# Kernel tuning notes

Hardware: AMD Instinct MI355X
Metric: run time of the kernel (lower is better)

Reference implementation:

```python
import jax, jax.numpy as jnp
import numpy as np

N_NODES = 100000
N_EDGES = 1600000
FEAT = 128
HID = 128
CLASSES = 10
GRAPHS = 64


def gcn_conv(x, W, b, src, dst, n):
    # PyG GCNConv: h = x @ W; add self-loops; symmetric deg^{-1/2} norm; scatter-add; + bias
    h = x @ W
    src_f = jnp.concatenate([src, jnp.arange(n, dtype=src.dtype)])
    dst_f = jnp.concatenate([dst, jnp.arange(n, dtype=dst.dtype)])
    deg = jax.ops.segment_sum(jnp.ones_like(dst_f, dtype=h.dtype), dst_f, num_segments=n)
    dinv = jax.lax.rsqrt(jnp.where(deg > 0, deg, 1.0))
    norm = dinv[src_f] * dinv[dst_f]              # [E+N]
    msg = h[src_f] * norm[:, None]                # gather + scale
    out = jax.ops.segment_sum(msg, dst_f, num_segments=n)  # scatter-add
    return out + b


def global_mean_pool(x, batch, num_graphs):
    s = jax.ops.segment_sum(x, batch, num_segments=num_graphs)
    cnt = jax.ops.segment_sum(jnp.ones_like(batch, dtype=x.dtype), batch, num_segments=num_graphs)
    return s / jnp.maximum(cnt, 1.0)[:, None]


def setup_inputs() -> dict:
    key = jax.random.key(0)
    ks = jax.random.split(key, 10)
    x = jax.random.normal(ks[0], (N_NODES, FEAT), dtype=jnp.float32)
    edge_index = jax.random.randint(ks[1], (2, N_EDGES), 0, N_NODES, dtype=jnp.int64)
    batch = jnp.sort(jax.random.randint(ks[2], (N_NODES,), 0, GRAPHS, dtype=jnp.int64))
    def glorot(k, fi, fo):
        s = float(np.sqrt(6.0 / (fi + fo)))
        return jax.random.uniform(k, (fi, fo), jnp.float32, -s, s)
    return {
        "x": x, "edge_index": edge_index, "batch": batch,
        "W1": glorot(ks[3], FEAT, HID), "b1": jnp.zeros((HID,), jnp.float32),
        "W2": glorot(ks[4], HID, HID), "b2": jnp.zeros((HID,), jnp.float32),
        "W3": glorot(ks[5], HID, HID), "b3": jnp.zeros((HID,), jnp.float32),
        "Wlin": glorot(ks[6], HID, CLASSES), "blin": jnp.zeros((CLASSES,), jnp.float32),
    }


def reference(x, edge_index, batch, W1, b1, W2, b2, W3, b3, Wlin, blin):
    src, dst = edge_index[0], edge_index[1]
    n = x.shape[0]
    h = jax.nn.relu(gcn_conv(x, W1, b1, src, dst, n))
    h = jax.nn.relu(gcn_conv(h, W2, b2, src, dst, n))
    h = gcn_conv(h, W3, b3, src, dst, n)
    emb = global_mean_pool(h, batch, GRAPHS)      # [GRAPHS, HID]
    # dropout(p=0.5) is identity in eval mode
    logits = emb @ Wlin + blin                    # [GRAPHS, CLASSES]
    return logits, jnp.squeeze(emb)
```

## Files before the change

### kernel.cpp

```cpp
#include <hip/hip_runtime.h>
#include <hip/hip_bf16.h>
#include <stdint.h>

typedef unsigned int uint32;
typedef __attribute__((ext_vector_type(8))) short short8;
typedef __attribute__((ext_vector_type(4))) float float4v;

#define FEAT 128
#define NGRAPH 64
#define SBLK 256
#define STHR 256
#define SSEG 2
#define GB   256
#define NBK  512

__device__ __forceinline__ float bf2f_lo(uint32 v) {
    union { uint32 i; float f; } u; u.i = v << 16; return u.f;
}
__device__ __forceinline__ float bf2f_hi(uint32 v) {
    union { uint32 i; float f; } u; u.i = v & 0xffff0000u; return u.f;
}
__device__ __forceinline__ unsigned short f2bf(float f) {
    uint32 u = __builtin_bit_cast(uint32, f);
    uint32 r = (u + 0x7fffu + ((u >> 16) & 1u)) >> 16;
    return (unsigned short)r;
}
__device__ __forceinline__ uint32 f2bf2(float lo, float hi) {
    return (uint32)f2bf(lo) | ((uint32)f2bf(hi) << 16);
}


__global__ void k_bhist(const int* __restrict__ dst, int* __restrict__ bhist, int E) {
    __shared__ int h[NBK];
    int t = threadIdx.x, blk = blockIdx.x;
    for (int b = t; b < NBK; b += 256) h[b] = 0;
    __syncthreads();
    int chunk = (E + GB - 1) / GB;
    int lo = blk * chunk, hi = min(lo + chunk, E);
    for (int e = lo + t; e < hi; e += 256)
        atomicAdd(&h[dst[e] >> 8], 1);
    __syncthreads();
    for (int b = t; b < NBK; b += 256) bhist[blk * NBK + b] = h[b];
}

__global__ void k_boffs(int* __restrict__ bhist, int* __restrict__ bbase) {
    __shared__ int sc[NBK];
    int t = threadIdx.x;
    int tot = 0;
    for (int blk = 0; blk < GB; blk++) {
        int v = bhist[blk * NBK + t];
        bhist[blk * NBK + t] = tot;
        tot += v;
    }
    sc[t] = tot;
    __syncthreads();
    for (int off = 1; off < NBK; off <<= 1) {
        int v = (t >= off) ? sc[t - off] : 0;
        __syncthreads();
        sc[t] += v;
        __syncthreads();
    }
    bbase[t] = sc[t] - tot;
    if (t == NBK - 1) bbase[NBK] = sc[t];
}

__global__ void k_bscat(const int* __restrict__ src, const int* __restrict__ dst,
                        const int* __restrict__ bhist, const int* __restrict__ bbase,
                        uint32* __restrict__ ebuf, int E) {
    __shared__ int cur[NBK];
    int t = threadIdx.x, blk = blockIdx.x;
    for (int b = t; b < NBK; b += 256) cur[b] = bbase[b] + bhist[blk * NBK + b];
    __syncthreads();
    int chunk = (E + GB - 1) / GB;
    int lo = blk * chunk, hi = min(lo + chunk, E);
    for (int e = lo + t; e < hi; e += 256) {
        int d = dst[e], s = src[e];
        int b = d >> 8;
        int p = atomicAdd(&cur[b], 1);
        ebuf[p] = ((uint32)s << 8) | (uint32)(d & 255);
    }
}

__global__ void k_count2(const uint32* __restrict__ ebuf, const int* __restrict__ bbase,
                         int* __restrict__ counts, int N) {
    __shared__ int h[256];
    int t = threadIdx.x, b = blockIdx.x;
    h[t] = 0;
    __syncthreads();
    int e0 = bbase[b], e1 = bbase[b + 1];
    for (int e = e0 + t; e < e1; e += 256)
        atomicAdd(&h[ebuf[e] & 255u], 1);
    __syncthreads();
    int node = b * 256 + t;
    if (node < N) counts[node] = h[t];
}

__global__ void k_fill2(const uint32* __restrict__ ebuf, const int* __restrict__ bbase,
                        const int* __restrict__ rowp, int* __restrict__ csrc, int N) {
    __shared__ int cur[256];
    int t = threadIdx.x, b = blockIdx.x;
    int node = b * 256 + t;
    cur[t] = (node < N) ? rowp[node] : 0;
    __syncthreads();
    int e0 = bbase[b], e1 = bbase[b + 1];
    for (int e = e0 + t; e < e1; e += 256) {
        uint32 v = ebuf[e];
        int p = atomicAdd(&cur[v & 255u], 1);
        csrc[p] = (int)(v >> 8);
    }
}

__global__ void k_dinv(const int* __restrict__ counts, float* __restrict__ dinv, int N) {
    int i = blockIdx.x * blockDim.x + threadIdx.x;
    if (i < N) dinv[i] = rsqrtf((float)counts[i] + 1.0f);
}

__global__ void k_scan_a(const int* __restrict__ counts, int* __restrict__ tbase,
                         int* __restrict__ bsum, int N) {
    __shared__ int sc[STHR];
    int t = threadIdx.x, b = blockIdx.x;
    int g = b * STHR + t;
    int lo = g * SSEG;
    int s = 0;
#pragma unroll
    for (int j = 0; j < SSEG; j++) {
        int i = lo + j;
        if (i < N) s += counts[i];
    }
    sc[t] = s;
    __syncthreads();
    for (int off = 1; off < STHR; off <<= 1) {
        int v = (t >= off) ? sc[t - off] : 0;
        __syncthreads();
        sc[t] += v;
        __syncthreads();
    }
    tbase[g] = sc[t] - s;
    if (t == STHR - 1) bsum[b] = sc[t];
}

__global__ void k_scan_b(const int* __restrict__ bsum, int* __restrict__ bbase2,
                         int* __restrict__ rowp, int N) {
    __shared__ int sc[SBLK];
    int t = threadIdx.x;
    int s = bsum[t];
    sc[t] = s;
    __syncthreads();
    for (int off = 1; off < SBLK; off <<= 1) {
        int v = (t >= off) ? sc[t - off] : 0;
        __syncthreads();
        sc[t] += v;
        __syncthreads();
    }
    bbase2[t] = sc[t] - s;
    if (t == SBLK - 1) rowp[N] = sc[t];
}

__global__ void k_scan_c(const int* __restrict__ counts, const int* __restrict__ tbase,
                         const int* __restrict__ bbase2, int* __restrict__ rowp, int N) {
    int t = threadIdx.x, b = blockIdx.x;
    int g = b * STHR + t;
    int base = bbase2[b] + tbase[g];
    int lo = g * SSEG;
#pragma unroll
    for (int j = 0; j < SSEG; j++) {
        int i = lo + j;
        if (i < N) { rowp[i] = base; base += counts[i]; }
    }
}

__global__ void k_cast(const float* __restrict__ X, uint32* __restrict__ Xb, long n2) {
    long i = (long)blockIdx.x * blockDim.x + threadIdx.x;
    long stride = (long)gridDim.x * blockDim.x;
    for (; i < n2; i += stride) {
        float2 v = *(const float2*)(X + 2 * i);
        Xb[i] = f2bf2(v.x, v.y);
    }
}

__global__ void k_wswz(const float* __restrict__ W, unsigned short* __restrict__ out) {
    int e = blockIdx.x * blockDim.x + threadIdx.x;
    if (e >= 2048) return;
    int kt = e >> 9, ct = (e >> 6) & 7, lane = e & 63;
    int krow = kt * 32 + (lane >> 4) * 8;
    int col = ct * 16 + (lane & 15);
#pragma unroll
    for (int j = 0; j < 8; j++)
        out[e * 8 + j] = f2bf(W[(krow + j) * FEAT + col]);
}

__global__ void k_gemm(const uint32* __restrict__ Xb,
                       const unsigned short* __restrict__ Wswz,
                       const float* __restrict__ dinv,
                       unsigned short* __restrict__ Hb, int N) {
    __shared__ unsigned short Wl[FEAT * FEAT];
    {
        const uint4* Wg = (const uint4*)Wswz;
        uint4* Ws = (uint4*)Wl;
        for (int i = threadIdx.x; i < 2048; i += 256) Ws[i] = Wg[i];
    }
    __syncthreads();

    int wave = threadIdx.x >> 6, lane = threadIdx.x & 63;
    int r0 = (blockIdx.x * 4 + wave) * 16;
    if (r0 >= N) return;
    int m = lane & 15, q = lane >> 4;

    int arow = r0 + m; if (arow >= N) arow = N - 1;
    const short8* Arow = (const short8*)((const unsigned short*)Xb + (long)arow * FEAT);
    short8 a0 = Arow[q + 0];
    short8 a1 = Arow[4 + q];
    short8 a2 = Arow[8 + q];
    short8 a3 = Arow[12 + q];

    const short8* Bl = (const short8*)Wl;
    float4v acc[8];
#pragma unroll
    for (int ct = 0; ct < 8; ct++) acc[ct] = (float4v){0.f, 0.f, 0.f, 0.f};

#pragma unroll
    for (int ct = 0; ct < 8; ct++) {
        acc[ct] = __builtin_amdgcn_mfma_f32_16x16x32_bf16(a0, Bl[(0 * 8 + ct) * 64 + lane], acc[ct], 0, 0, 0);
        acc[ct] = __builtin_amdgcn_mfma_f32_16x16x32_bf16(a1, Bl[(1 * 8 + ct) * 64 + lane], acc[ct], 0, 0, 0);
        acc[ct] = __builtin_amdgcn_mfma_f32_16x16x32_bf16(a2, Bl[(2 * 8 + ct) * 64 + lane], acc[ct], 0, 0, 0);
        acc[ct] = __builtin_amdgcn_mfma_f32_16x16x32_bf16(a3, Bl[(3 * 8 + ct) * 64 + lane], acc[ct], 0, 0, 0);
    }

    float ds[4];
#pragma unroll
    for (int reg = 0; reg < 4; reg++) {
        int row = r0 + q * 4 + reg;
        ds[reg] = (row < N) ? dinv[row] : 0.f;
    }
#pragma unroll
    for (int ct = 0; ct < 8; ct++) {
#pragma unroll
        for (int reg = 0; reg < 4; reg++) {
            int row = r0 + q * 4 + reg;
            if (row < N) Hb[(long)row * FEAT + ct * 16 + m] = f2bf(acc[ct][reg] * ds[reg]);
        }
    }
}

__global__ void k_agg(const uint32* __restrict__ Hb,
                      const int* __restrict__ rowp, const int* __restrict__ csrc,
                      const float* __restrict__ dinv, const float* __restrict__ bias,
                      uint32* __restrict__ OUTb, int N, int relu) {
    int wave = threadIdx.x >> 6, lane = threadIdx.x & 63;
    int i = blockIdx.x * 4 + wave;
    if (i >= N) return;
    float di = dinv[i];
    uint32 hv = Hb[(long)i * 64 + lane];
    float ax = bf2f_lo(hv), ay = bf2f_hi(hv);
    int e0 = rowp[i], e1 = rowp[i + 1];
    int e = e0;
    for (; e + 8 <= e1; e += 8) {
        int   s[8];
        uint32 h[8];
#pragma unroll
        for (int j = 0; j < 8; j++) s[j] = csrc[e + j];
#pragma unroll
        for (int j = 0; j < 8; j++) h[j] = Hb[(long)s[j] * 64 + lane];
#pragma unroll
        for (int j = 0; j < 8; j++) {
            ax += bf2f_lo(h[j]);
            ay += bf2f_hi(h[j]);
        }
    }
    {
        int   s[8];
        uint32 h[8];
        int r = e1 - e;
#pragma unroll
        for (int j = 0; j < 8; j++)
            if (j < r) s[j] = csrc[e + j];
#pragma unroll
        for (int j = 0; j < 8; j++)
            if (j < r) h[j] = Hb[(long)s[j] * 64 + lane];
#pragma unroll
        for (int j = 0; j < 8; j++)
            if (j < r) { ax += bf2f_lo(h[j]); ay += bf2f_hi(h[j]); }
    }
    ax = ax * di + bias[2 * lane];
    ay = ay * di + bias[2 * lane + 1];
    if (relu) { ax = fmaxf(ax, 0.f); ay = fmaxf(ay, 0.f); }
    OUTb[(long)i * 64 + lane] = f2bf2(ax, ay);
}

__global__ void k_pool(const uint32* __restrict__ Gb, const int* __restrict__ batch,
                       float* __restrict__ pool, int* __restrict__ cntg, int N) {
    int t = threadIdx.x;
    int nb = gridDim.x;
    int chunk = (N + nb - 1) / nb;
    int lo = blockIdx.x * chunk, hi = min(lo + chunk, N);
    if (lo >= hi) return;
    float ax = 0.f, ay = 0.f;
    int cnt = 0;
    int cg = batch[lo];
    for (int i = lo; i < hi; i++) {
        int g = batch[i];
        if (g != cg) {
            atomicAdd(&pool[cg * FEAT + 2 * t], ax);
            atomicAdd(&pool[cg * FEAT + 2 * t + 1], ay);
            if (t == 0) atomicAdd(&cntg[cg], cnt);
            ax = ay = 0.f; cnt = 0; cg = g;
        }
        uint32 v = Gb[(long)i * 64 + t];
        ax += bf2f_lo(v); ay += bf2f_hi(v);
        cnt++;
    }
    atomicAdd(&pool[cg * FEAT + 2 * t], ax);
    atomicAdd(&pool[cg * FEAT + 2 * t + 1], ay);
    if (t == 0) atomicAdd(&cntg[cg], cnt);
}

__global__ void k_final(const float* __restrict__ pool, const int* __restrict__ cntg,
                        const float* __restrict__ Wlin, const float* __restrict__ blin,
                        float* __restrict__ out) {
    __shared__ float es[FEAT];
    int g = blockIdx.x, t = threadIdx.x;
    float c = (float)max(cntg[g], 1);
    float e = pool[g * FEAT + t] / c;
    es[t] = e;
    out[NGRAPH * 10 + g * FEAT + t] = e;
    __syncthreads();
    if (t < 10) {
        float a = blin[t];
        for (int k = 0; k < FEAT; k++)
            a += es[k] * Wlin[k * 10 + t];
        out[g * 10 + t] = a;
    }
}

extern "C" void kernel_launch(void* const* d_in, const int* in_sizes, int n_in,
                              void* d_out, int out_size, void* d_ws, size_t ws_size,
                              hipStream_t stream) {
    const float* x    = (const float*)d_in[0];
    const int*   ei   = (const int*)d_in[1];
    const int*   batch= (const int*)d_in[2];
    const float* W1   = (const float*)d_in[3];
    const float* b1   = (const float*)d_in[4];
    const float* W2   = (const float*)d_in[5];
    const float* b2   = (const float*)d_in[6];
    const float* W3   = (const float*)d_in[7];
    const float* b3   = (const float*)d_in[8];
    const float* Wlin = (const float*)d_in[9];
    const float* blin = (const float*)d_in[10];

    const int N = in_sizes[2];
    const int E = in_sizes[1] / 2;
    const int* src = ei;
    const int* dst = ei + E;
    const int NB = (N + 255) >> 8;

    char* w = (char*)d_ws;
    auto take = [&](size_t bytes) {
        char* p = w;
        w += (bytes + 255) & ~(size_t)255;
        return p;
    };
    int*    counts = (int*)   take((size_t)N * 4);
    float*  dinv   = (float*) take((size_t)N * 4);
    int*    rowp   = (int*)   take((size_t)(N + 1) * 4);
    int*    csrc   = (int*)   take((size_t)E * 4);
    uint32* ebuf   = (uint32*)take((size_t)E * 4);
    int*    bhist  = (int*)   take((size_t)GB * NBK * 4);
    int*    bbase  = (int*)   take((size_t)(NBK + 1) * 4);
    uint32* xb     = (uint32*)take((size_t)N * FEAT * 2);
    uint32* hbuf   = (uint32*)take((size_t)N * FEAT * 2);
    uint32* gbuf   = (uint32*)take((size_t)N * FEAT * 2);
    unsigned short* w1s = (unsigned short*)take(FEAT * FEAT * 2);
    unsigned short* w2s = (unsigned short*)take(FEAT * FEAT * 2);
    unsigned short* w3s = (unsigned short*)take(FEAT * FEAT * 2);
    float*  pool   = (float*) take((size_t)NGRAPH * FEAT * 4);
    int*    cntg   = (int*)   take((size_t)NGRAPH * 4);
    int*    tbase  = (int*)   take((size_t)SBLK * STHR * 4);
    int*    bsum   = (int*)   take((size_t)SBLK * 4);
    int*    bbase2 = (int*)   take((size_t)SBLK * 4);
    (void)ws_size; (void)n_in; (void)out_size;

    const int bn = (N + 255) / 256;

    hipMemsetAsync(pool, 0, (size_t)NGRAPH * FEAT * 4, stream);
    hipMemsetAsync(cntg, 0, (size_t)NGRAPH * 4, stream);

    k_bhist <<<GB, 256, 0, stream>>>(dst, bhist, E);
    k_boffs <<<1, NBK, 0, stream>>>(bhist, bbase);
    k_bscat <<<GB, 256, 0, stream>>>(src, dst, bhist, bbase, ebuf, E);
    k_count2<<<NB, 256, 0, stream>>>(ebuf, bbase, counts, N);
    k_dinv  <<<bn, 256, 0, stream>>>(counts, dinv, N);
    k_scan_a<<<SBLK, STHR, 0, stream>>>(counts, tbase, bsum, N);
    k_scan_b<<<1, SBLK, 0, stream>>>(bsum, bbase2, rowp, N);
    k_scan_c<<<SBLK, STHR, 0, stream>>>(counts, tbase, bbase2, rowp, N);
    k_fill2 <<<NB, 256, 0, stream>>>(ebuf, bbase, rowp, csrc, N);

    k_cast<<<2048, 256, 0, stream>>>(x, xb, (long)N * FEAT / 2);
    k_wswz<<<8, 256, 0, stream>>>(W1, w1s);
    k_wswz<<<8, 256, 0, stream>>>(W2, w2s);
    k_wswz<<<8, 256, 0, stream>>>(W3, w3s);

    const int gemm_blocks = (N + 63) / 64;
    const int agg_blocks  = (N + 3) / 4;

    k_gemm<<<gemm_blocks, 256, 0, stream>>>(xb, w1s, dinv, (unsigned short*)hbuf, N);
    k_agg <<<agg_blocks, 256, 0, stream>>>(hbuf, rowp, csrc, dinv, b1, gbuf, N, 1);
    k_gemm<<<gemm_blocks, 256, 0, stream>>>(gbuf, w2s, dinv, (unsigned short*)hbuf, N);
    k_agg <<<agg_blocks, 256, 0, stream>>>(hbuf, rowp, csrc, dinv, b2, gbuf, N, 1);
    k_gemm<<<gemm_blocks, 256, 0, stream>>>(gbuf, w3s, dinv, (unsigned short*)hbuf, N);
    k_agg <<<agg_blocks, 256, 0, stream>>>(hbuf, rowp, csrc, dinv, b3, gbuf, N, 0);

    k_pool <<<1024, 64, 0, stream>>>(gbuf, batch, pool, cntg, N);
    k_final<<<NGRAPH, 128, 0, stream>>>(pool, cntg, Wlin, blin, (float*)d_out);
}
```

Before: 491.5 us.

## Fuse dinv, cast and weight-swizzle kernels; widen aggregation gathers to 8-byte loads

Computes dinv inside the count kernel, removes the separate fp32-to-bf16 cast by converting x inside the first GEMM, and merges the three weight swizzle launches into one. The aggregation kernel now splits each wave into two halves that each gather a different neighbour using 8-byte loads, then combines the halves with a cross-lane shuffle. The goal is fewer launches, no extra pass over x, and more memory-level parallelism in the gather. In exchange the first GEMM reads fp32 rows directly, and only half the lanes do the final write.

```diff
diff --git a/kernel.cpp b/kernel.cpp
--- a/kernel.cpp
+++ b/kernel.cpp
@@ -28,7 +28,6 @@
 __device__ __forceinline__ uint32 f2bf2(float lo, float hi) {
     return (uint32)f2bf(lo) | ((uint32)f2bf(hi) << 16);
 }
-
 
 __global__ void k_bhist(const int* __restrict__ dst, int* __restrict__ bhist, int E) {
     __shared__ int h[NBK];
@@ -82,7 +81,7 @@
 }
 
 __global__ void k_count2(const uint32* __restrict__ ebuf, const int* __restrict__ bbase,
-                         int* __restrict__ counts, int N) {
+                         int* __restrict__ counts, float* __restrict__ dinv, int N) {
     __shared__ int h[256];
     int t = threadIdx.x, b = blockIdx.x;
     h[t] = 0;
@@ -92,7 +91,10 @@
         atomicAdd(&h[ebuf[e] & 255u], 1);
     __syncthreads();
     int node = b * 256 + t;
-    if (node < N) counts[node] = h[t];
+    if (node < N) {
+        counts[node] = h[t];
+        dinv[node] = rsqrtf((float)h[t] + 1.0f);
+    }
 }
 
 __global__ void k_fill2(const uint32* __restrict__ ebuf, const int* __restrict__ bbase,
@@ -108,11 +110,6 @@
         int p = atomicAdd(&cur[v & 255u], 1);
         csrc[p] = (int)(v >> 8);
     }
-}
-
-__global__ void k_dinv(const int* __restrict__ counts, float* __restrict__ dinv, int N) {
-    int i = blockIdx.x * blockDim.x + threadIdx.x;
-    if (i < N) dinv[i] = rsqrtf((float)counts[i] + 1.0f);
 }
 
 __global__ void k_scan_a(const int* __restrict__ counts, int* __restrict__ tbase,
@@ -169,18 +166,13 @@
     }
 }
 
-__global__ void k_cast(const float* __restrict__ X, uint32* __restrict__ Xb, long n2) {
-    long i = (long)blockIdx.x * blockDim.x + threadIdx.x;
-    long stride = (long)gridDim.x * blockDim.x;
-    for (; i < n2; i += stride) {
-        float2 v = *(const float2*)(X + 2 * i);
-        Xb[i] = f2bf2(v.x, v.y);
-    }
-}
-
-__global__ void k_wswz(const float* __restrict__ W, unsigned short* __restrict__ out) {
-    int e = blockIdx.x * blockDim.x + threadIdx.x;
-    if (e >= 2048) return;
+__global__ void k_wswz3(const float* __restrict__ W1, const float* __restrict__ W2,
+                        const float* __restrict__ W3, unsigned short* __restrict__ o1,
+                        unsigned short* __restrict__ o2, unsigned short* __restrict__ o3) {
+    int wid = blockIdx.x >> 3;
+    const float* W = (wid == 0) ? W1 : (wid == 1) ? W2 : W3;
+    unsigned short* out = (wid == 0) ? o1 : (wid == 1) ? o2 : o3;
+    int e = (blockIdx.x & 7) * 256 + threadIdx.x;
     int kt = e >> 9, ct = (e >> 6) & 7, lane = e & 63;
     int krow = kt * 32 + (lane >> 4) * 8;
     int col = ct * 16 + (lane & 15);
@@ -189,7 +181,8 @@
         out[e * 8 + j] = f2bf(W[(krow + j) * FEAT + col]);
 }
 
-__global__ void k_gemm(const uint32* __restrict__ Xb,
+template <bool F32IN>
+__global__ void k_gemm(const void* __restrict__ Xp,
                        const unsigned short* __restrict__ Wswz,
                        const float* __restrict__ dinv,
                        unsigned short* __restrict__ Hb, int N) {
@@ -207,11 +200,25 @@
     int m = lane & 15, q = lane >> 4;
 
     int arow = r0 + m; if (arow >= N) arow = N - 1;
-    const short8* Arow = (const short8*)((const unsigned short*)Xb + (long)arow * FEAT);
-    short8 a0 = Arow[q + 0];
-    short8 a1 = Arow[4 + q];
-    short8 a2 = Arow[8 + q];
-    short8 a3 = Arow[12 + q];
+    short8 a[4];
+    if (F32IN) {
+        const float* Ar = (const float*)Xp + (long)arow * FEAT;
+#pragma unroll
+        for (int kt = 0; kt < 4; kt++) {
+            float4 u = *(const float4*)(Ar + kt * 32 + q * 8);
+            float4 v = *(const float4*)(Ar + kt * 32 + q * 8 + 4);
+            short8 t;
+            t[0] = (short)f2bf(u.x); t[1] = (short)f2bf(u.y);
+            t[2] = (short)f2bf(u.z); t[3] = (short)f2bf(u.w);
+            t[4] = (short)f2bf(v.x); t[5] = (short)f2bf(v.y);
+            t[6] = (short)f2bf(v.z); t[7] = (short)f2bf(v.w);
+            a[kt] = t;
+        }
+    } else {
+        const short8* Ar = (const short8*)((const unsigned short*)Xp + (long)arow * FEAT);
+#pragma unroll
+        for (int kt = 0; kt < 4; kt++) a[kt] = Ar[kt * 4 + q];
+    }
 
     const short8* Bl = (const short8*)Wl;
     float4v acc[8];
@@ -220,10 +227,10 @@
 
 #pragma unroll
     for (int ct = 0; ct < 8; ct++) {
-        acc[ct] = __builtin_amdgcn_mfma_f32_16x16x32_bf16(a0, Bl[(0 * 8 + ct) * 64 + lane], acc[ct], 0, 0, 0);
-        acc[ct] = __builtin_amdgcn_mfma_f32_16x16x32_bf16(a1, Bl[(1 * 8 + ct) * 64 + lane], acc[ct], 0, 0, 0);
-        acc[ct] = __builtin_amdgcn_mfma_f32_16x16x32_bf16(a2, Bl[(2 * 8 + ct) * 64 + lane], acc[ct], 0, 0, 0);
-        acc[ct] = __builtin_amdgcn_mfma_f32_16x16x32_bf16(a3, Bl[(3 * 8 + ct) * 64 + lane], acc[ct], 0, 0, 0);
+        acc[ct] = __builtin_amdgcn_mfma_f32_16x16x32_bf16(a[0], Bl[(0 * 8 + ct) * 64 + lane], acc[ct], 0, 0, 0);
+        acc[ct] = __builtin_amdgcn_mfma_f32_16x16x32_bf16(a[1], Bl[(1 * 8 + ct) * 64 + lane], acc[ct], 0, 0, 0);
+        acc[ct] = __builtin_amdgcn_mfma_f32_16x16x32_bf16(a[2], Bl[(2 * 8 + ct) * 64 + lane], acc[ct], 0, 0, 0);
+        acc[ct] = __builtin_amdgcn_mfma_f32_16x16x32_bf16(a[3], Bl[(3 * 8 + ct) * 64 + lane], acc[ct], 0, 0, 0);
     }
 
     float ds[4];
@@ -249,42 +256,64 @@
     int wave = threadIdx.x >> 6, lane = threadIdx.x & 63;
     int i = blockIdx.x * 4 + wave;
     if (i >= N) return;
-    float di = dinv[i];
-    uint32 hv = Hb[(long)i * 64 + lane];
-    float ax = bf2f_lo(hv), ay = bf2f_hi(hv);
+    int f = lane & 31, half = lane >> 5;
+    const uint2* H2 = (const uint2*)Hb;
+    float a0 = 0.f, a1 = 0.f, a2 = 0.f, a3 = 0.f;
     int e0 = rowp[i], e1 = rowp[i + 1];
     int e = e0;
-    for (; e + 8 <= e1; e += 8) {
-        int   s[8];
-        uint32 h[8];
-#pragma unroll
-        for (int j = 0; j < 8; j++) s[j] = csrc[e + j];
-#pragma unroll
-        for (int j = 0; j < 8; j++) h[j] = Hb[(long)s[j] * 64 + lane];
+    for (; e + 16 <= e1; e += 16) {
+        int  s[8];
+        uint2 h[8];
+#pragma unroll
+        for (int j = 0; j < 8; j++) s[j] = csrc[e + 2 * j + half];
+#pragma unroll
+        for (int j = 0; j < 8; j++) h[j] = H2[(long)s[j] * 32 + f];
 #pragma unroll
         for (int j = 0; j < 8; j++) {
-            ax += bf2f_lo(h[j]);
-            ay += bf2f_hi(h[j]);
+            a0 += bf2f_lo(h[j].x); a1 += bf2f_hi(h[j].x);
+            a2 += bf2f_lo(h[j].y); a3 += bf2f_hi(h[j].y);
         }
     }
     {
-        int   s[8];
-        uint32 h[8];
         int r = e1 - e;
+        int  s[8];
+        uint2 h[8];
+#pragma unroll
+        for (int j = 0; j < 8; j++) {
+            int idx = 2 * j + half;
+            if (idx < r) s[j] = csrc[e + idx];
+        }
 #pragma unroll
         for (int j = 0; j < 8; j++)
-            if (j < r) s[j] = csrc[e + j];
+            if (2 * j + half < r) h[j] = H2[(long)s[j] * 32 + f];
 #pragma unroll
         for (int j = 0; j < 8; j++)
-            if (j < r) h[j] = Hb[(long)s[j] * 64 + lane];
-#pragma unroll
-        for (int j = 0; j < 8; j++)
-            if (j < r) { ax += bf2f_lo(h[j]); ay += bf2f_hi(h[j]); }
-    }
-    ax = ax * di + bias[2 * lane];
-    ay = ay * di + bias[2 * lane + 1];
-    if (relu) { ax = fmaxf(ax, 0.f); ay = fmaxf(ay, 0.f); }
-    OUTb[(long)i * 64 + lane] = f2bf2(ax, ay);
+            if (2 * j + half < r) {
+                a0 += bf2f_lo(h[j].x); a1 += bf2f_hi(h[j].x);
+                a2 += bf2f_lo(h[j].y); a3 += bf2f_hi(h[j].y);
+            }
+    }
+    a0 += __shfl_xor(a0, 32);
+    a1 += __shfl_xor(a1, 32);
+    a2 += __shfl_xor(a2, 32);
+    a3 += __shfl_xor(a3, 32);
+    if (half == 0) {
+        uint2 hv = H2[(long)i * 32 + f];
+        a0 += bf2f_lo(hv.x); a1 += bf2f_hi(hv.x);
+        a2 += bf2f_lo(hv.y); a3 += bf2f_hi(hv.y);
+        float di = dinv[i];
+        float4 bb = ((const float4*)bias)[f];
+        a0 = a0 * di + bb.x; a1 = a1 * di + bb.y;
+        a2 = a2 * di + bb.z; a3 = a3 * di + bb.w;
+        if (relu) {
+            a0 = fmaxf(a0, 0.f); a1 = fmaxf(a1, 0.f);
+            a2 = fmaxf(a2, 0.f); a3 = fmaxf(a3, 0.f);
+        }
+        uint2 o;
+        o.x = f2bf2(a0, a1);
+        o.y = f2bf2(a2, a3);
+        ((uint2*)OUTb)[(long)i * 32 + f] = o;
+    }
 }
 
 __global__ void k_pool(const uint32* __restrict__ Gb, const int* __restrict__ batch,
@@ -366,7 +395,6 @@
     uint32* ebuf   = (uint32*)take((size_t)E * 4);
     int*    bhist  = (int*)   take((size_t)GB * NBK * 4);
     int*    bbase  = (int*)   take((size_t)(NBK + 1) * 4);
-    uint32* xb     = (uint32*)take((size_t)N * FEAT * 2);
     uint32* hbuf   = (uint32*)take((size_t)N * FEAT * 2);
     uint32* gbuf   = (uint32*)take((size_t)N * FEAT * 2);
     unsigned short* w1s = (unsigned short*)take(FEAT * FEAT * 2);
@@ -379,34 +407,28 @@
     int*    bbase2 = (int*)   take((size_t)SBLK * 4);
     (void)ws_size; (void)n_in; (void)out_size;
 
-    const int bn = (N + 255) / 256;
-
     hipMemsetAsync(pool, 0, (size_t)NGRAPH * FEAT * 4, stream);
     hipMemsetAsync(cntg, 0, (size_t)NGRAPH * 4, stream);
 
     k_bhist <<<GB, 256, 0, stream>>>(dst, bhist, E);
     k_boffs <<<1, NBK, 0, stream>>>(bhist, bbase);
     k_bscat <<<GB, 256, 0, stream>>>(src, dst, bhist, bbase, ebuf, E);
-    k_count2<<<NB, 256, 0, stream>>>(ebuf, bbase, counts, N);
-    k_dinv  <<<bn, 256, 0, stream>>>(counts, dinv, N);
+    k_count2<<<NB, 256, 0, stream>>>(ebuf, bbase, counts, dinv, N);
     k_scan_a<<<SBLK, STHR, 0, stream>>>(counts, tbase, bsum, N);
     k_scan_b<<<1, SBLK, 0, stream>>>(bsum, bbase2, rowp, N);
     k_scan_c<<<SBLK, STHR, 0, stream>>>(counts, tbase, bbase2, rowp, N);
     k_fill2 <<<NB, 256, 0, stream>>>(ebuf, bbase, rowp, csrc, N);
 
-    k_cast<<<2048, 256, 0, stream>>>(x, xb, (long)N * FEAT / 2);
-    k_wswz<<<8, 256, 0, stream>>>(W1, w1s);
-    k_wswz<<<8, 256, 0, stream>>>(W2, w2s);
-    k_wswz<<<8, 256, 0, stream>>>(W3, w3s);
+    k_wswz3<<<24, 256, 0, stream>>>(W1, W2, W3, w1s, w2s, w3s);
 
     const int gemm_blocks = (N + 63) / 64;
     const int agg_blocks  = (N + 3) / 4;
 
-    k_gemm<<<gemm_blocks, 256, 0, stream>>>(xb, w1s, dinv, (unsigned short*)hbuf, N);
+    k_gemm<true> <<<gemm_blocks, 256, 0, stream>>>(x, w1s, dinv, (unsigned short*)hbuf, N);
     k_agg <<<agg_blocks, 256, 0, stream>>>(hbuf, rowp, csrc, dinv, b1, gbuf, N, 1);
-    k_gemm<<<gemm_blocks, 256, 0, stream>>>(gbuf, w2s, dinv, (unsigned short*)hbuf, N);
+    k_gemm<false><<<gemm_blocks, 256, 0, stream>>>(gbuf, w2s, dinv, (unsigned short*)hbuf, N);
     k_agg <<<agg_blocks, 256, 0, stream>>>(hbuf, rowp, csrc, dinv, b2, gbuf, N, 1);
-    k_gemm<<<gemm_blocks, 256, 0, stream>>>(gbuf, w3s, dinv, (unsigned short*)hbuf, N);
+    k_gemm<false><<<gemm_blocks, 256, 0, stream>>>(gbuf, w3s, dinv, (unsigned short*)hbuf, N);
     k_agg <<<agg_blocks, 256, 0, stream>>>(hbuf, rowp, csrc, dinv, b3, gbuf, N, 0);
 
     k_pool <<<1024, 64, 0, stream>>>(gbuf, batch, pool, cntg, N);
```

Result: faster. 464.7 us (-5.5%).
